# Kernel optimization log

Measured on AMD Instinct MI355X. Metric: run time of the kernel, lower is better.

Reference implementation:

```python
import jax, jax.numpy as jnp
import numpy as np

HIDDEN = 1024  # must match init_kwargs hidden_size


def setup_inputs() -> dict:
    key = jax.random.key(0)
    k1, k2 = jax.random.split(key)
    B, SQ, SKV, D = 4, 4096, 4096, HIDDEN
    query = jax.random.normal(k1, (B, SQ, D), dtype=jnp.float32)
    key_value_states = jax.random.normal(k2, (B, SKV, D), dtype=jnp.float32)
    attention_mask = jnp.zeros((B, 1, SKV), dtype=jnp.float32)
    return {
        "query": query,
        "key_value_states": key_value_states,
        "attention_mask": attention_mask,
        "layer_idx": 0,
    }


def reference(query, key_value_states, attention_mask, layer_idx):
    # compression_rate = 1.0 + layer_idx/12*3 ; layer_idx=0 -> rate 1.0 (no compression)
    scale = 1.0 / jnp.sqrt(jnp.asarray(HIDDEN, dtype=query.dtype))
    # scores: [B, Sq, Skv]
    scores = jnp.einsum("bqd,bkd->bqk", query, key_value_states) * scale
    scores = scores + attention_mask
    attn = jax.nn.softmax(scores, axis=-1)
    # dropout is identity (eval / p=0)
    out = jnp.einsum("bqk,bkd->bqd", attn, key_value_states)
    return out, attn
```

## Files before the change

### kernel.cpp

```cpp
#include <hip/hip_runtime.h>
#include <hip/hip_fp16.h>
#include <stdint.h>

#define B_   4
#define SQ_  4096
#define SKV_ 4096
#define D_   1024

typedef __attribute__((ext_vector_type(4))) float f32x4;
typedef __attribute__((ext_vector_type(8))) short bf8_t;

__device__ __forceinline__ unsigned short f2bf(float f) {
    unsigned u = __float_as_uint(f);
    u += 0x7fff + ((u >> 16) & 1);
    return (unsigned short)(u >> 16);
}

__device__ __forceinline__ void gload_lds16(const void* g, void* l) {
    __builtin_amdgcn_global_load_lds(
        (const __attribute__((address_space(1))) unsigned int*)g,
        (__attribute__((address_space(3))) unsigned int*)l,
        16, 0, 0);
}

__global__ void cvt_f32_bf16_kernel(const float* __restrict__ in,
                                    unsigned short* __restrict__ out, int n4) {
    int stride = gridDim.x * blockDim.x;
    for (int i = blockIdx.x * blockDim.x + threadIdx.x; i < n4; i += stride) {
        float4 v = ((const float4*)in)[i];
        ushort4 o;
        o.x = f2bf(v.x); o.y = f2bf(v.y); o.z = f2bf(v.z); o.w = f2bf(v.w);
        ((ushort4*)out)[i] = o;
    }
}

__global__ void cvtkv_kernel(const float* __restrict__ V,
                             unsigned short* __restrict__ Kbf,
                             unsigned short* __restrict__ VT) {
    __shared__ float tile[32][33];
    int b = blockIdx.z;
    const float* Vb = V + (size_t)b * SKV_ * D_;
    unsigned short* Kb = Kbf + (size_t)b * SKV_ * D_;
    unsigned short* VTb = VT + (size_t)b * D_ * SKV_;
    int d0 = blockIdx.x * 32, k0 = blockIdx.y * 32;
    int x = threadIdx.x, y = threadIdx.y;
    #pragma unroll
    for (int i = 0; i < 4; ++i) {
        float v = Vb[(size_t)(k0 + y + i * 8) * D_ + d0 + x];
        tile[y + i * 8][x] = v;
        Kb[(size_t)(k0 + y + i * 8) * D_ + d0 + x] = f2bf(v);
    }
    __syncthreads();
    #pragma unroll
    for (int i = 0; i < 4; ++i)
        VTb[(size_t)(d0 + y + i * 8) * SKV_ + k0 + x] = f2bf(tile[x][y + i * 8]);
}

template<int MODE>
__global__ __launch_bounds__(256, 3) void gemm128_kernel(
    const unsigned short* __restrict__ A, int lda, size_t strideA,
    const unsigned short* __restrict__ Bm, int ldb, size_t strideB,
    void* __restrict__ Cv, int ldc, size_t strideC,
    int K, float scale, const float* __restrict__ mask,
    const float* __restrict__ sums)
{
    __shared__ __align__(16) unsigned char smem[32768];

    const int tid  = threadIdx.x;
    const int lane = tid & 63, wid = tid >> 6;
    const int wr = wid >> 1, wc = wid & 1;

    int lin  = blockIdx.y * gridDim.x + blockIdx.x;
    int q8   = (gridDim.x * gridDim.y) >> 3;
    int lin2 = (lin & 7) * q8 + (lin >> 3);
    int bn = lin2 % gridDim.x, bm = lin2 / gridDim.x;
    int bz = blockIdx.z;

    const char* Ab = (const char*)(A + (size_t)bz * strideA);
    const char* Bb = (const char*)(Bm + (size_t)bz * strideB);
    const int ldaB = lda * 2, ldbB = ldb * 2;

    const char* aSrc[4]; const char* bSrc[4]; int dstOff[4];
    #pragma unroll
    for (int q = 0; q < 4; ++q) {
        int o = q * 256 + tid;
        int g = o & 3, r = (o >> 2) & 127, kk = o >> 9;
        aSrc[q] = Ab + (size_t)(bm * 128 + r) * ldaB + kk * 64 + g * 16;
        bSrc[q] = Bb + (size_t)(bn * 128 + r) * ldbB + kk * 64 + g * 16;
        dstOff[q] = o * 16;
    }
    char* ldsA = (char*)smem;
    char* ldsB = (char*)smem + 16384;

    const int rbase = (lane & 15) * 64 + (lane >> 4) * 16;
    const char* aRd = ldsA + wr * 4096 + rbase;
    const char* bRd = ldsB + wc * 4096 + rbase;

    f32x4 acc[4][4] = {};

    for (int k0 = 0; k0 < K; k0 += 64) {
        #pragma unroll
        for (int q = 0; q < 4; ++q) gload_lds16(aSrc[q], ldsA + dstOff[q]);
        #pragma unroll
        for (int q = 0; q < 4; ++q) gload_lds16(bSrc[q], ldsB + dstOff[q]);
        #pragma unroll
        for (int q = 0; q < 4; ++q) { aSrc[q] += 128; bSrc[q] += 128; }
        __syncthreads();
        #pragma unroll
        for (int kk = 0; kk < 2; ++kk) {
            bf8_t af[4], bfv[4];
            #pragma unroll
            for (int m = 0; m < 4; ++m) af[m]  = *(const bf8_t*)(aRd + kk * 8192 + m * 1024);
            #pragma unroll
            for (int n = 0; n < 4; ++n) bfv[n] = *(const bf8_t*)(bRd + kk * 8192 + n * 1024);
            #pragma unroll
            for (int m = 0; m < 4; ++m)
                #pragma unroll
                for (int n = 0; n < 4; ++n)
                    acc[m][n] = __builtin_amdgcn_mfma_f32_16x16x32_bf16(
                        af[m], bfv[n], acc[m][n], 0, 0, 0);
        }
        __syncthreads();
    }

    const int row0 = bm * 128 + wr * 64 + (lane >> 4) * 4;
    const int col0 = bn * 128 + wc * 64 + (lane & 15);
    if (MODE == 0) {
        unsigned short* Ch = (unsigned short*)Cv + (size_t)bz * strideC;
        const float* maskb = mask + (size_t)bz * SKV_;
        #pragma unroll
        for (int n = 0; n < 4; ++n) {
            int col = col0 + n * 16;
            float mk = maskb[col];
            #pragma unroll
            for (int m = 0; m < 4; ++m) {
                int row = row0 + m * 16;
                #pragma unroll
                for (int r = 0; r < 4; ++r) {
                    float v = __expf(fminf(acc[m][n][r] * scale + mk, 80.0f));
                    Ch[(size_t)(row + r) * ldc + col] = f2bf(v);
                }
            }
        }
    } else {
        float* Cf = (float*)Cv + (size_t)bz * strideC;
        const float* sb = sums + (size_t)bz * SQ_;
        float rinv[4][4];
        #pragma unroll
        for (int m = 0; m < 4; ++m)
            #pragma unroll
            for (int r = 0; r < 4; ++r)
                rinv[m][r] = 1.0f / sb[row0 + m * 16 + r];
        #pragma unroll
        for (int n = 0; n < 4; ++n) {
            int col = col0 + n * 16;
            #pragma unroll
            for (int m = 0; m < 4; ++m) {
                int row = row0 + m * 16;
                #pragma unroll
                for (int r = 0; r < 4; ++r)
                    Cf[(size_t)(row + r) * ldc + col] = acc[m][n][r] * rinv[m][r];
            }
        }
    }
}

__global__ __launch_bounds__(256) void normalize_kernel(const unsigned short* __restrict__ p,
                                                        float* __restrict__ attn,
                                                        float* __restrict__ sums) {
    __shared__ __align__(16) float buf[SKV_];
    __shared__ float red[4];
    size_t row = blockIdx.x;
    const unsigned short* pr = p + row * SKV_;
    float* ao = attn + row * SKV_;
    int t = threadIdx.x;

    float lsum = 0.f;
    for (int i = t * 8; i < SKV_; i += 2048) {
        uint4 hv = *(const uint4*)(pr + i);
        float v0 = __uint_as_float(hv.x << 16), v1 = __uint_as_float(hv.x & 0xffff0000u);
        float v2 = __uint_as_float(hv.y << 16), v3 = __uint_as_float(hv.y & 0xffff0000u);
        float v4 = __uint_as_float(hv.z << 16), v5 = __uint_as_float(hv.z & 0xffff0000u);
        float v6 = __uint_as_float(hv.w << 16), v7 = __uint_as_float(hv.w & 0xffff0000u);
        buf[i+0] = v0; buf[i+1] = v1; buf[i+2] = v2; buf[i+3] = v3;
        buf[i+4] = v4; buf[i+5] = v5; buf[i+6] = v6; buf[i+7] = v7;
        lsum += ((v0 + v1) + (v2 + v3)) + ((v4 + v5) + (v6 + v7));
    }
    #pragma unroll
    for (int o = 32; o; o >>= 1) lsum += __shfl_down(lsum, o);
    if ((t & 63) == 0) red[t >> 6] = lsum;
    __syncthreads();
    float sum = (red[0] + red[1]) + (red[2] + red[3]);
    float rinv = 1.0f / sum;

    for (int i = t * 8; i < SKV_; i += 2048) {
        float4 v0 = *(const float4*)&buf[i];
        float4 v1 = *(const float4*)&buf[i + 4];
        v0.x *= rinv; v0.y *= rinv; v0.z *= rinv; v0.w *= rinv;
        v1.x *= rinv; v1.y *= rinv; v1.z *= rinv; v1.w *= rinv;
        *(float4*)(ao + i) = v0;
        *(float4*)(ao + i + 4) = v1;
    }
    if (t == 0) sums[row] = sum;
}

__global__ __launch_bounds__(256) void softmax_f32_kernel(float* __restrict__ scores) {
    __shared__ __align__(16) float buf[SKV_];
    __shared__ float red[4];
    size_t row = blockIdx.x;
    float* p = scores + row * SKV_;
    int t = threadIdx.x;
    float lmax = -3.4e38f;
    for (int i = t * 4; i < SKV_; i += 1024) {
        float4 v = *(const float4*)(p + i);
        *(float4*)&buf[i] = v;
        lmax = fmaxf(fmaxf(lmax, fmaxf(v.x, v.y)), fmaxf(v.z, v.w));
    }
    #pragma unroll
    for (int o = 32; o; o >>= 1) lmax = fmaxf(lmax, __shfl_down(lmax, o));
    if ((t & 63) == 0) red[t >> 6] = lmax;
    __syncthreads();
    float rmax = fmaxf(fmaxf(red[0], red[1]), fmaxf(red[2], red[3]));
    __syncthreads();
    float lsum = 0.f;
    for (int i = t * 4; i < SKV_; i += 1024) {
        float4 v = *(const float4*)&buf[i];
        v.x = __expf(v.x - rmax); v.y = __expf(v.y - rmax);
        v.z = __expf(v.z - rmax); v.w = __expf(v.w - rmax);
        *(float4*)&buf[i] = v;
        lsum += (v.x + v.y) + (v.z + v.w);
    }
    #pragma unroll
    for (int o = 32; o; o >>= 1) lsum += __shfl_down(lsum, o);
    if ((t & 63) == 0) red[t >> 6] = lsum;
    __syncthreads();
    float rinv = 1.0f / ((red[0] + red[1]) + (red[2] + red[3]));
    for (int i = t * 4; i < SKV_; i += 1024) {
        float4 v = *(const float4*)&buf[i];
        v.x *= rinv; v.y *= rinv; v.z *= rinv; v.w *= rinv;
        *(float4*)(p + i) = v;
    }
}

__global__ void naive_nt_kernel(const float* __restrict__ A, const float* __restrict__ Bm,
                                float* __restrict__ C, const float* __restrict__ mask,
                                int N, int K, float scale) {
    __shared__ float As[16][16], Bs[16][16];
    int b = blockIdx.z;
    const float* Ab = A + (size_t)b * SQ_ * K;
    const float* Bb = Bm + (size_t)b * N * K;
    float* Cb = C + (size_t)b * SQ_ * N;
    int tx = threadIdx.x, ty = threadIdx.y;
    int m = blockIdx.y * 16 + ty, n = blockIdx.x * 16 + tx;
    float acc = 0.f;
    for (int k0 = 0; k0 < K; k0 += 16) {
        As[ty][tx] = Ab[(size_t)m * K + k0 + tx];
        Bs[ty][tx] = Bb[(size_t)(blockIdx.x * 16 + ty) * K + k0 + tx];
        __syncthreads();
        #pragma unroll
        for (int kk = 0; kk < 16; ++kk) acc += As[ty][kk] * Bs[tx][kk];
        __syncthreads();
    }
    Cb[(size_t)m * N + n] = acc * scale + (mask ? mask[(size_t)b * SKV_ + n] : 0.f);
}

__global__ void naive_nn_kernel(const float* __restrict__ A, const float* __restrict__ Bm,
                                float* __restrict__ C, int N, int K) {
    __shared__ float As[16][16], Bs[16][17];
    int b = blockIdx.z;
    const float* Ab = A + (size_t)b * SQ_ * K;
    const float* Bb = Bm + (size_t)b * K * N;
    float* Cb = C + (size_t)b * SQ_ * N;
    int tx = threadIdx.x, ty = threadIdx.y;
    int m = blockIdx.y * 16 + ty, n = blockIdx.x * 16 + tx;
    float acc = 0.f;
    for (int k0 = 0; k0 < K; k0 += 16) {
        As[ty][tx] = Ab[(size_t)m * K + k0 + tx];
        Bs[ty][tx] = Bb[(size_t)(k0 + ty) * N + n];
        __syncthreads();
        #pragma unroll
        for (int kk = 0; kk < 16; ++kk) acc += As[ty][kk] * Bs[kk][tx];
        __syncthreads();
    }
    Cb[(size_t)m * N + n] = acc;
}

extern "C" void kernel_launch(void* const* d_in, const int* in_sizes, int n_in,
                              void* d_out, int out_size, void* d_ws, size_t ws_size,
                              hipStream_t stream) {
    const float* q    = (const float*)d_in[0];
    const float* kv   = (const float*)d_in[1];
    const float* mask = (const float*)d_in[2];

    float* out  = (float*)d_out;
    float* attn = out + (size_t)B_ * SQ_ * D_;
    const float scale = 0.03125f;

    size_t nQ    = (size_t)B_ * SQ_ * D_;
    size_t nKV   = (size_t)B_ * SKV_ * D_;
    size_t nAttn = (size_t)B_ * SQ_ * SKV_;
    size_t need  = (nQ + nKV + nKV + nAttn) * 2;

    if (ws_size >= need) {
        unsigned short* qbf  = (unsigned short*)d_ws;
        unsigned short* kbf  = qbf + nQ;
        unsigned short* vtbf = kbf + nKV;
        unsigned short* s2   = vtbf + nKV;
        float* sums = (float*)qbf;

        cvt_f32_bf16_kernel<<<2048, 256, 0, stream>>>(q, qbf, (int)(nQ / 4));
        cvtkv_kernel<<<dim3(D_ / 32, SKV_ / 32, B_), dim3(32, 8), 0, stream>>>(kv, kbf, vtbf);

        gemm128_kernel<0><<<dim3(SKV_ / 128, SQ_ / 128, B_), 256, 0, stream>>>(
            qbf, D_, (size_t)SQ_ * D_,
            kbf, D_, (size_t)SKV_ * D_,
            (void*)s2, SKV_, (size_t)SQ_ * SKV_,
            D_, scale, mask, nullptr);

        normalize_kernel<<<B_ * SQ_, 256, 0, stream>>>(s2, attn, sums);

        gemm128_kernel<1><<<dim3(D_ / 128, SQ_ / 128, B_), 256, 0, stream>>>(
            s2, SKV_, (size_t)SQ_ * SKV_,
            vtbf, SKV_, (size_t)D_ * SKV_,
            (void*)out, D_, (size_t)SQ_ * D_,
            SKV_, 1.0f, nullptr, sums);
    } else {
        naive_nt_kernel<<<dim3(SKV_ / 16, SQ_ / 16, B_), dim3(16, 16), 0, stream>>>(
            q, kv, attn, mask, SKV_, D_, scale);
        softmax_f32_kernel<<<B_ * SQ_, 256, 0, stream>>>(attn);
        naive_nn_kernel<<<dim3(D_ / 16, SQ_ / 16, B_), dim3(16, 16), 0, stream>>>(
            attn, kv, out, D_, SKV_);
    }
}
```

Measured before the change: 472.2 us.

## Fuse softmax normalization and attn write into the PV GEMM epilogue

Removes the separate normalize kernel. Row sums of the unnormalized exponentials are now computed inside the PV GEMM by an extra MFMA per row-fragment against a vector of bf16 ones. The blocks in column 0 then reload their 128 rows of bf16 probabilities, scale them by the reciprocal sums and write the fp32 attn matrix. This saves a kernel launch and a separate full pass over the probability buffer. In exchange it adds about 25% more MFMA work in the second GEMM and puts all attn stores on only one eighth of the blocks, which can create a long tail.

Result: slower. 612.3 us (+29.7%).

```diff
diff --git a/kernel.cpp b/kernel.cpp
--- a/kernel.cpp
+++ b/kernel.cpp
@@ -62,7 +62,7 @@
     const unsigned short* __restrict__ Bm, int ldb, size_t strideB,
     void* __restrict__ Cv, int ldc, size_t strideC,
     int K, float scale, const float* __restrict__ mask,
-    const float* __restrict__ sums)
+    float* __restrict__ attn)
 {
     __shared__ __align__(16) unsigned char smem[32768];
 
@@ -97,6 +97,10 @@
     const char* bRd = ldsB + wc * 4096 + rbase;
 
     f32x4 acc[4][4] = {};
+    f32x4 acc_s[4] = {};
+    bf8_t ones;
+    #pragma unroll
+    for (int j = 0; j < 8; ++j) ones[j] = (short)0x3F80;
 
     for (int k0 = 0; k0 < K; k0 += 64) {
         #pragma unroll
@@ -119,6 +123,12 @@
                 for (int n = 0; n < 4; ++n)
                     acc[m][n] = __builtin_amdgcn_mfma_f32_16x16x32_bf16(
                         af[m], bfv[n], acc[m][n], 0, 0, 0);
+            if (MODE == 1) {
+                #pragma unroll
+                for (int m = 0; m < 4; ++m)
+                    acc_s[m] = __builtin_amdgcn_mfma_f32_16x16x32_bf16(
+                        af[m], ones, acc_s[m], 0, 0, 0);
+            }
         }
         __syncthreads();
     }
@@ -144,13 +154,12 @@
         }
     } else {
         float* Cf = (float*)Cv + (size_t)bz * strideC;
-        const float* sb = sums + (size_t)bz * SQ_;
         float rinv[4][4];
         #pragma unroll
         for (int m = 0; m < 4; ++m)
             #pragma unroll
             for (int r = 0; r < 4; ++r)
-                rinv[m][r] = 1.0f / sb[row0 + m * 16 + r];
+                rinv[m][r] = 1.0f / acc_s[m][r];
         #pragma unroll
         for (int n = 0; n < 4; ++n) {
             int col = col0 + n * 16;
@@ -162,46 +171,38 @@
                     Cf[(size_t)(row + r) * ldc + col] = acc[m][n][r] * rinv[m][r];
             }
         }
-    }
-}
-
-__global__ __launch_bounds__(256) void normalize_kernel(const unsigned short* __restrict__ p,
-                                                        float* __restrict__ attn,
-                                                        float* __restrict__ sums) {
-    __shared__ __align__(16) float buf[SKV_];
-    __shared__ float red[4];
-    size_t row = blockIdx.x;
-    const unsigned short* pr = p + row * SKV_;
-    float* ao = attn + row * SKV_;
-    int t = threadIdx.x;
-
-    float lsum = 0.f;
-    for (int i = t * 8; i < SKV_; i += 2048) {
-        uint4 hv = *(const uint4*)(pr + i);
-        float v0 = __uint_as_float(hv.x << 16), v1 = __uint_as_float(hv.x & 0xffff0000u);
-        float v2 = __uint_as_float(hv.y << 16), v3 = __uint_as_float(hv.y & 0xffff0000u);
-        float v4 = __uint_as_float(hv.z << 16), v5 = __uint_as_float(hv.z & 0xffff0000u);
-        float v6 = __uint_as_float(hv.w << 16), v7 = __uint_as_float(hv.w & 0xffff0000u);
-        buf[i+0] = v0; buf[i+1] = v1; buf[i+2] = v2; buf[i+3] = v3;
-        buf[i+4] = v4; buf[i+5] = v5; buf[i+6] = v6; buf[i+7] = v7;
-        lsum += ((v0 + v1) + (v2 + v3)) + ((v4 + v5) + (v6 + v7));
-    }
-    #pragma unroll
-    for (int o = 32; o; o >>= 1) lsum += __shfl_down(lsum, o);
-    if ((t & 63) == 0) red[t >> 6] = lsum;
-    __syncthreads();
-    float sum = (red[0] + red[1]) + (red[2] + red[3]);
-    float rinv = 1.0f / sum;
-
-    for (int i = t * 8; i < SKV_; i += 2048) {
-        float4 v0 = *(const float4*)&buf[i];
-        float4 v1 = *(const float4*)&buf[i + 4];
-        v0.x *= rinv; v0.y *= rinv; v0.z *= rinv; v0.w *= rinv;
-        v1.x *= rinv; v1.y *= rinv; v1.z *= rinv; v1.w *= rinv;
-        *(float4*)(ao + i) = v0;
-        *(float4*)(ao + i + 4) = v1;
-    }
-    if (t == 0) sums[row] = sum;
+        float* rs = (float*)smem;
+        __syncthreads();
+        if (wc == 0 && (lane & 15) == 0) {
+            #pragma unroll
+            for (int m = 0; m < 4; ++m)
+                #pragma unroll
+                for (int r = 0; r < 4; ++r)
+                    rs[wr * 64 + m * 16 + (lane >> 4) * 4 + r] = rinv[m][r];
+        }
+        __syncthreads();
+        if (attn != nullptr && bn == 0) {
+            const unsigned short* pB = (const unsigned short*)Ab + (size_t)(bm * 128) * lda;
+            float* attnB = attn + (size_t)bz * SQ_ * SKV_ + (size_t)(bm * 128) * SKV_;
+            for (int idx = tid; idx < 128 * 512; idx += 256) {
+                int row = idx >> 9, c = (idx & 511) * 8;
+                uint4 hv = *(const uint4*)(pB + (size_t)row * lda + c);
+                float rv = rs[row];
+                float4 w0, w1;
+                w0.x = __uint_as_float(hv.x << 16) * rv;
+                w0.y = __uint_as_float(hv.x & 0xffff0000u) * rv;
+                w0.z = __uint_as_float(hv.y << 16) * rv;
+                w0.w = __uint_as_float(hv.y & 0xffff0000u) * rv;
+                w1.x = __uint_as_float(hv.z << 16) * rv;
+                w1.y = __uint_as_float(hv.z & 0xffff0000u) * rv;
+                w1.z = __uint_as_float(hv.w << 16) * rv;
+                w1.w = __uint_as_float(hv.w & 0xffff0000u) * rv;
+                float* ap = attnB + (size_t)row * SKV_ + c;
+                *(float4*)ap = w0;
+                *(float4*)(ap + 4) = w1;
+            }
+        }
+    }
 }
 
 __global__ __launch_bounds__(256) void softmax_f32_kernel(float* __restrict__ scores) {
@@ -306,7 +307,6 @@
         unsigned short* kbf  = qbf + nQ;
         unsigned short* vtbf = kbf + nKV;
         unsigned short* s2   = vtbf + nKV;
-        float* sums = (float*)qbf;
 
         cvt_f32_bf16_kernel<<<2048, 256, 0, stream>>>(q, qbf, (int)(nQ / 4));
         cvtkv_kernel<<<dim3(D_ / 32, SKV_ / 32, B_), dim3(32, 8), 0, stream>>>(kv, kbf, vtbf);
@@ -317,13 +317,11 @@
             (void*)s2, SKV_, (size_t)SQ_ * SKV_,
             D_, scale, mask, nullptr);
 
-        normalize_kernel<<<B_ * SQ_, 256, 0, stream>>>(s2, attn, sums);
-
         gemm128_kernel<1><<<dim3(D_ / 128, SQ_ / 128, B_), 256, 0, stream>>>(
             s2, SKV_, (size_t)SQ_ * SKV_,
             vtbf, SKV_, (size_t)D_ * SKV_,
             (void*)out, D_, (size_t)SQ_ * D_,
-            SKV_, 1.0f, nullptr, sums);
+            SKV_, 1.0f, nullptr, attn);
     } else {
         naive_nt_kernel<<<dim3(SKV_ / 16, SQ_ / 16, B_), dim3(16, 16), 0, stream>>>(
             q, kv, attn, mask, SKV_, D_, scale);
```
